# Kernel tuning notes

Hardware: AMD Instinct MI355X
Metric: run time of the kernel (lower is better)

## Reference

```python
import jax, jax.numpy as jnp
import numpy as np

NP = 16   # attention heads
HN = 128  # head dim (kv_channels)
MASK_VAL = -10000.0  # attention_mask_func fill value in TE


def setup_inputs() -> dict:
    key = jax.random.key(0)
    ks = jax.random.split(key, 5)
    S, B, H = 2048, 1, 2048
    return {
        "hidden_states": jax.random.normal(ks[0], (S, B, H), jnp.float32),
        "w_qkv": jax.random.normal(ks[1], (3 * H, H), jnp.float32) * 0.02,
        "b_qkv": jax.random.normal(ks[2], (3 * H,), jnp.float32) * 0.02,
        "w_proj": jax.random.normal(ks[3], (H, H), jnp.float32) * 0.02,
        "b_proj": jax.random.normal(ks[4], (H,), jnp.float32) * 0.02,
        "attention_mask": jnp.zeros((1, 1, S, S), dtype=bool),
    }


def reference(hidden_states, w_qkv, b_qkv, w_proj, b_proj, attention_mask):
    S, B, H = hidden_states.shape
    # fused QKV GEMM: [s, b, 3h]
    qkv = jnp.einsum("sbh,oh->sbo", hidden_states, w_qkv) + b_qkv
    qkv = qkv.reshape(S, B, NP, 3 * HN)
    q, k, v = jnp.split(qkv, 3, axis=-1)  # each [s, b, np, hn]

    # BMM1: full [b, np, sq, sk] score matrix (naive unfused attention)
    norm_factor = jnp.asarray(np.sqrt(HN), q.dtype)
    scores = jnp.einsum("sbnh,tbnh->bnst", q, k) / norm_factor

    # causal mask (attn_mask_type='causal'); provided mask OR'd in (zeros here)
    causal = jnp.triu(jnp.ones((S, S), dtype=bool), 1)
    mask = jnp.logical_or(causal, attention_mask[0, 0])
    scores = jnp.where(mask, jnp.asarray(MASK_VAL, scores.dtype), scores)

    # softmax in fp32 (apply_query_key_layer_scaling forces fp32 softmax)
    probs = jax.nn.softmax(scores.astype(jnp.float32), axis=-1).astype(q.dtype)
    # dropout p=0.0 -> identity

    # BMM2 + merge heads -> [s, b, h]
    ctx = jnp.einsum("bnst,tbnh->sbnh", probs, v).reshape(S, B, H)

    # output projection (bias returned separately, return_bias=True)
    out = jnp.einsum("sbh,oh->sbo", ctx, w_proj)
    return out, b_proj
```

## Files before the change

kernel.cpp:

```cpp
#include <hip/hip_runtime.h>
#include <math.h>

#define S_LEN   2048
#define H_DIM   2048
#define QKV_LD  6144
#define N_HEADS 16
#define HEAD_DIM 128

typedef __attribute__((ext_vector_type(8))) short short8;
typedef __attribute__((ext_vector_type(4))) float f32x4;
typedef __attribute__((ext_vector_type(16))) float f32x16;
typedef unsigned short ushort_t;

__device__ __forceinline__ ushort_t f2bf(float x) {
    unsigned int u = __float_as_uint(x);
    u = (u + 0x7fffu + ((u >> 16) & 1u)) >> 16;
    return (ushort_t)u;
}

__device__ __forceinline__ unsigned cvtpk_bf16(float a, float b) {
    unsigned r;
    asm("v_cvt_pk_bf16_f32 %0, %1, %2" : "=v"(r) : "v"(a), "v"(b));
    return r;
}

__device__ __forceinline__ void plswap(unsigned &a, unsigned &b) {
    typedef unsigned uv2 __attribute__((ext_vector_type(2)));
    uv2 r = __builtin_amdgcn_permlane32_swap(a, b, false, false);
    a = r[0]; b = r[1];
}

#define GLOBAL_LOAD_LDS16(gp, lp)                                              \
    __builtin_amdgcn_global_load_lds(                                          \
        (const __attribute__((address_space(1))) void*)(gp),                   \
        (__attribute__((address_space(3))) void*)(lp), 16, 0, 0)

#define MKFRAG(P, base, out) {                                                 \
    unsigned wa = cvtpk_bf16(P[(base)+0], P[(base)+1]);                        \
    unsigned wb = cvtpk_bf16(P[(base)+4], P[(base)+5]);                        \
    unsigned wc = cvtpk_bf16(P[(base)+2], P[(base)+3]);                        \
    unsigned wd = cvtpk_bf16(P[(base)+6], P[(base)+7]);                        \
    plswap(wa, wb); plswap(wc, wd);                                            \
    union { unsigned u[4]; short8 s; } fu;                                     \
    fu.u[0] = wa; fu.u[1] = wc; fu.u[2] = wb; fu.u[3] = wd;                    \
    out = fu.s; }

__global__ __launch_bounds__(256) void cvt_bf16(const float* __restrict__ src,
                                                ushort_t* __restrict__ dst) {
    const int i = (blockIdx.x * 256 + threadIdx.x) * 8;
    float4 a = *(const float4*)(src + i);
    float4 b = *(const float4*)(src + i + 4);
    short8 v;
    v[0] = f2bf(a.x); v[1] = f2bf(a.y); v[2] = f2bf(a.z); v[3] = f2bf(a.w);
    v[4] = f2bf(b.x); v[5] = f2bf(b.y); v[6] = f2bf(b.z); v[7] = f2bf(b.w);
    *(short8*)(dst + i) = v;
}

template <bool BIAS, bool OUT_BF16>
__global__ __launch_bounds__(256)
void gemm_bf16_nt(const ushort_t* __restrict__ A, const ushort_t* __restrict__ B,
                  const float* __restrict__ bias, void* __restrict__ Cout,
                  int M, int N, int K) {
    __shared__ __align__(16) ushort_t As[128 * 64];
    __shared__ __align__(16) ushort_t Bs[128 * 64];

    const int tid  = threadIdx.x;
    const int lane = tid & 63;
    const int w    = tid >> 6;
    const int wr   = w >> 1, wc = w & 1;
    const int m0   = blockIdx.y << 7;
    const int n0   = blockIdx.x << 7;
    const int frow = lane & 15;
    const int fk16 = (lane >> 4) << 4;

    f32x4 acc[4][4];
    #pragma unroll
    for (int i = 0; i < 4; i++)
        #pragma unroll
        for (int j = 0; j < 4; j++) acc[i][j] = (f32x4){0.f, 0.f, 0.f, 0.f};

    for (int k0 = 0; k0 < K; k0 += 64) {
        __syncthreads();
        #pragma unroll
        for (int i = 0; i < 4; i++) {
            const int off = (i * 256 + tid) * 8;
            const int r   = off >> 6;
            const int cb  = ((off & 63) * 2) ^ ((r & 7) << 4);
            GLOBAL_LOAD_LDS16((const char*)(A + (size_t)(m0 + r) * K + k0) + cb,
                              (char*)As + off * 2);
            GLOBAL_LOAD_LDS16((const char*)(B + (size_t)(n0 + r) * K + k0) + cb,
                              (char*)Bs + off * 2);
        }
        __syncthreads();
        #pragma unroll
        for (int kk = 0; kk < 2; kk++) {
            short8 a[4], b[4];
            #pragma unroll
            for (int mi = 0; mi < 4; mi++) {
                const int row = wr * 64 + mi * 16 + frow;
                const int cb  = (kk * 64 + fk16) ^ ((row & 7) << 4);
                a[mi] = *(const short8*)((const char*)As + row * 128 + cb);
            }
            #pragma unroll
            for (int ni = 0; ni < 4; ni++) {
                const int row = wc * 64 + ni * 16 + frow;
                const int cb  = (kk * 64 + fk16) ^ ((row & 7) << 4);
                b[ni] = *(const short8*)((const char*)Bs + row * 128 + cb);
            }
            #pragma unroll
            for (int mi = 0; mi < 4; mi++)
                #pragma unroll
                for (int ni = 0; ni < 4; ni++)
                    acc[mi][ni] = __builtin_amdgcn_mfma_f32_16x16x32_bf16(
                        a[mi], b[ni], acc[mi][ni], 0, 0, 0);
        }
    }

    const int crow0 = (lane >> 4) * 4;
    const int ccol  = lane & 15;
    #pragma unroll
    for (int mi = 0; mi < 4; mi++) {
        #pragma unroll
        for (int ni = 0; ni < 4; ni++) {
            const int col = n0 + wc * 64 + ni * 16 + ccol;
            const float bv = BIAS ? bias[col] : 0.f;
            #pragma unroll
            for (int r = 0; r < 4; r++) {
                const int row = m0 + wr * 64 + mi * 16 + crow0 + r;
                const float v = acc[mi][ni][r] + bv;
                if (OUT_BF16)
                    ((ushort_t*)Cout)[(size_t)row * N + col] = f2bf(v);
                else
                    ((float*)Cout)[(size_t)row * N + col] = v;
            }
        }
    }
}

__global__ __launch_bounds__(128)
void attn_mfma2(const ushort_t* __restrict__ qkv, ushort_t* __restrict__ ctx)
{
    __shared__ __align__(16) ushort_t Ks[2][64 * 128];
    __shared__ __align__(16) ushort_t Vt[2][128 * 72];

    const int tid  = threadIdx.x;
    const int lane = tid & 63;
    const int w    = tid >> 6;
    const int b    = blockIdx.x;
    const int head = blockIdx.y;
    const int l31  = lane & 31;
    const int hi   = lane >> 5;
    const size_t hbase = (size_t)head * 384;
    const ushort_t* kbase = qkv + hbase + 128;
    const ushort_t* vbase = qkv + hbase + 256;
    const int kq = tid & 15;
    const int dc = tid >> 4;

    short8 vreg[8];

    auto stage_k = [&](int kt, ushort_t* dst) {
        const int krow0 = kt << 6;
        #pragma unroll
        for (int i = 0; i < 8; i++) {
            const int off  = (i * 128 + tid) * 8;
            const int r    = off >> 7;
            const int slot = (off & 127) >> 3;
            const int sb   = (slot ^ (r & 15)) << 4;
            GLOBAL_LOAD_LDS16(
                (const char*)(kbase + (size_t)(krow0 + r) * QKV_LD) + sb,
                (char*)dst + off * 2);
        }
    };
    auto load_v = [&](int kt) {
        const int k0 = kt << 6;
        #pragma unroll
        for (int kk = 0; kk < 4; kk++)
            #pragma unroll
            for (int h2 = 0; h2 < 2; h2++)
                vreg[kk * 2 + h2] = *(const short8*)(vbase +
                    (size_t)(k0 + 4 * kq + kk) * QKV_LD + dc * 16 + h2 * 8);
    };
    auto write_vt = [&](ushort_t* dst) {
        #pragma unroll
        for (int j = 0; j < 16; j++) {
            const int h2 = j >> 3, e = j & 7;
            unsigned lo = (unsigned)(unsigned short)vreg[0 + h2][e] |
                          ((unsigned)(unsigned short)vreg[2 + h2][e] << 16);
            unsigned hh = (unsigned)(unsigned short)vreg[4 + h2][e] |
                          ((unsigned)(unsigned short)vreg[6 + h2][e] << 16);
            unsigned long long v64 =
                (unsigned long long)lo | ((unsigned long long)hh << 32);
            *(unsigned long long*)(dst + (dc * 16 + j) * 72 + 4 * kq) = v64;
        }
    };

    #pragma unroll 1
    for (int phase = 0; phase < 2; phase++) {
        const int qt = (phase == 0) ? (2 * b + w) : (63 - 2 * b - w);
        const int nt = (phase == 0) ? (b + 1) : (32 - b);
        const int q  = qt * 32 + l31;

        short8 qf[8];
        const ushort_t* qrow = qkv + (size_t)q * QKV_LD + hbase;
        #pragma unroll
        for (int ks = 0; ks < 8; ks++)
            qf[ks] = *(const short8*)(qrow + ks * 16 + hi * 8);

        f32x16 accO[4];
        #pragma unroll
        for (int dt = 0; dt < 4; dt++)
            #pragma unroll
            for (int i = 0; i < 16; i++) accO[dt][i] = 0.f;
        float m_run = -INFINITY, l_run = 0.f;

        stage_k(0, Ks[0]);
        load_v(0);
        __syncthreads();
        write_vt(Vt[0]);
        __syncthreads();

        for (int kt = 0; kt < nt; kt++) {
            const int cur = kt & 1;
            const ushort_t* Kc = Ks[cur];
            const ushort_t* Vc = Vt[cur];
            const bool pre = (kt + 1 < nt);
            if (pre) { stage_k(kt + 1, Ks[cur ^ 1]); load_v(kt + 1); }

            f32x16 s0, s1;
            #pragma unroll
            for (int i = 0; i < 16; i++) { s0[i] = 0.f; s1[i] = 0.f; }
            __builtin_amdgcn_s_setprio(1);
            #pragma unroll
            for (int ks = 0; ks < 8; ks++) {
                const int sb = (((2 * ks + hi) ^ (l31 & 15)) << 4);
                short8 kf0 = *(const short8*)((const char*)Kc + l31 * 256 + sb);
                short8 kf1 = *(const short8*)((const char*)Kc + (32 + l31) * 256 + sb);
                s0 = __builtin_amdgcn_mfma_f32_32x32x16_bf16(kf0, qf[ks], s0, 0, 0, 0);
                s1 = __builtin_amdgcn_mfma_f32_32x32x16_bf16(kf1, qf[ks], s1, 0, 0, 0);
            }
            __builtin_amdgcn_s_setprio(0);

            const float norm = 0.08838834764831843f;
            const int k0g = kt * 64;
            float p0[16], p1[16];
            #pragma unroll
            for (int r = 0; r < 16; r++) {
                const int kp = (r & 3) + 8 * (r >> 2) + 4 * hi;
                float v0 = s0[r] * norm;
                float v1 = s1[r] * norm;
                if (kt == nt - 1) {
                    if (k0g + kp > q)      v0 = -INFINITY;
                    if (k0g + 32 + kp > q) v1 = -INFINITY;
                }
                p0[r] = v0; p1[r] = v1;
            }
            float mx = fmaxf(p0[0], p1[0]);
            #pragma unroll
            for (int r = 1; r < 16; r++) mx = fmaxf(mx, fmaxf(p0[r], p1[r]));
            mx = fmaxf(mx, __shfl_xor(mx, 32));
            const float mnew = fmaxf(m_run, mx);
            float ps = 0.f;
            #pragma unroll
            for (int r = 0; r < 16; r++) {
                p0[r] = __expf(p0[r] - mnew);
                p1[r] = __expf(p1[r] - mnew);
                ps += p0[r] + p1[r];
            }
            ps += __shfl_xor(ps, 32);
            const float sc = __expf(m_run - mnew);
            l_run = l_run * sc + ps;
            m_run = mnew;
            #pragma unroll
            for (int dt = 0; dt < 4; dt++)
                #pragma unroll
                for (int i = 0; i < 16; i++) accO[dt][i] *= sc;

            short8 pf[4];
            MKFRAG(p0, 0, pf[0]); MKFRAG(p0, 8, pf[1]);
            MKFRAG(p1, 0, pf[2]); MKFRAG(p1, 8, pf[3]);

            if (pre) write_vt(Vt[cur ^ 1]);

            __builtin_amdgcn_s_setprio(1);
            #pragma unroll
            for (int dt = 0; dt < 4; dt++)
                #pragma unroll
                for (int ks = 0; ks < 4; ks++) {
                    short8 vf = *(const short8*)(Vc + (dt * 32 + l31) * 72 +
                                                 ks * 16 + hi * 8);
                    accO[dt] = __builtin_amdgcn_mfma_f32_32x32x16_bf16(
                        vf, pf[ks], accO[dt], 0, 0, 0);
                }
            __builtin_amdgcn_s_setprio(0);
            __syncthreads();
        }

        const float inv = 1.f / l_run;
        ushort_t* crow = ctx + (size_t)q * H_DIM + head * HEAD_DIM;
        #pragma unroll
        for (int dblk = 0; dblk < 8; dblk++) {
            const int dt = dblk >> 1;
            const int base = (dblk & 1) * 8;
            unsigned wa = cvtpk_bf16(accO[dt][base + 0] * inv, accO[dt][base + 1] * inv);
            unsigned wb = cvtpk_bf16(accO[dt][base + 4] * inv, accO[dt][base + 5] * inv);
            unsigned wc = cvtpk_bf16(accO[dt][base + 2] * inv, accO[dt][base + 3] * inv);
            unsigned wd = cvtpk_bf16(accO[dt][base + 6] * inv, accO[dt][base + 7] * inv);
            plswap(wa, wb); plswap(wc, wd);
            union { unsigned u[4]; short8 s; } fu;
            fu.u[0] = wa; fu.u[1] = wc; fu.u[2] = wb; fu.u[3] = wd;
            *(short8*)(crow + dblk * 16 + hi * 8) = fu.s;
        }
    }
}

__global__ __launch_bounds__(256) void copy_bias(const float* __restrict__ b,
                                                 float* __restrict__ out) {
    const int i = blockIdx.x * 256 + threadIdx.x;
    if (i < H_DIM) out[i] = b[i];
}

extern "C" void kernel_launch(void* const* d_in, const int* in_sizes, int n_in,
                              void* d_out, int out_size, void* d_ws, size_t ws_size,
                              hipStream_t stream) {
    const float* hidden = (const float*)d_in[0];
    const float* w_qkv  = (const float*)d_in[1];
    const float* b_qkv  = (const float*)d_in[2];
    const float* w_proj = (const float*)d_in[3];
    const float* b_proj = (const float*)d_in[4];
    float* out = (float*)d_out;

    ushort_t* qkvb = (ushort_t*)d_ws;
    ushort_t* bufB = qkvb + (size_t)S_LEN * QKV_LD;
    ushort_t* bufC = bufB + (size_t)S_LEN * H_DIM;

    cvt_bf16<<<dim3((S_LEN * H_DIM) / 2048), 256, 0, stream>>>(hidden, bufB);
    cvt_bf16<<<dim3((QKV_LD * H_DIM) / 2048), 256, 0, stream>>>(w_qkv, bufC);

    gemm_bf16_nt<true, true><<<dim3(QKV_LD / 128, S_LEN / 128), 256, 0, stream>>>(
        bufB, bufC, b_qkv, qkvb, S_LEN, QKV_LD, H_DIM);

    cvt_bf16<<<dim3((H_DIM * H_DIM) / 2048), 256, 0, stream>>>(w_proj, bufC);

    attn_mfma2<<<dim3(16, N_HEADS), 128, 0, stream>>>(qkvb, bufB);

    gemm_bf16_nt<false, false><<<dim3(H_DIM / 128, S_LEN / 128), 256, 0, stream>>>(
        bufB, bufC, nullptr, out, S_LEN, H_DIM, H_DIM);

    copy_bias<<<dim3((H_DIM + 255) / 256), 256, 0, stream>>>(
        b_proj, out + (size_t)S_LEN * H_DIM);
}
```

Measured before the change: 356.2 us.

## Pre-transpose V, triple-buffer async K/V staging in attention, shrink proj GEMM tile

A separate kernel now transposes V into a per-head [d, s] buffer in workspace. The attention kernel can then load both K and V tiles straight into LDS with async global-to-LDS copies, instead of loading V into registers and transposing it in shared memory. The attention loop uses a three-stage ring buffer with explicit vmcnt waits and raw barriers, so two tiles are prefetched ahead of compute, and its grid is reordered to head-major. The output projection GEMM gets a templated BM=64 tile, doubling its block count for better CU occupancy. In exchange there is an extra kernel launch, an extra pass over V through memory, and more LDS per attention block.

```diff
diff --git a/kernel.cpp b/kernel.cpp
--- a/kernel.cpp
+++ b/kernel.cpp
@@ -56,48 +56,82 @@
     *(short8*)(dst + i) = v;
 }
 
-template <bool BIAS, bool OUT_BF16>
+__global__ __launch_bounds__(256)
+void vt_transpose(const ushort_t* __restrict__ qkv, ushort_t* __restrict__ vt) {
+    __shared__ ushort_t T[64 * 72];
+    const int tid  = threadIdx.x;
+    const int s0   = blockIdx.x << 6;
+    const int d0   = blockIdx.y << 6;
+    const int head = blockIdx.z;
+    const ushort_t* src = qkv + (size_t)head * 384 + 256;
+    #pragma unroll
+    for (int j = 0; j < 2; j++) {
+        const int idx = j * 256 + tid;
+        const int r = idx >> 3, c = idx & 7;
+        *(short8*)&T[r * 72 + c * 8] =
+            *(const short8*)(src + (size_t)(s0 + r) * QKV_LD + d0 + c * 8);
+    }
+    __syncthreads();
+    #pragma unroll
+    for (int j = 0; j < 2; j++) {
+        const int idx = j * 256 + tid;
+        const int dr = idx >> 3, sc = idx & 7;
+        short8 v;
+        #pragma unroll
+        for (int e = 0; e < 8; e++) v[e] = T[(sc * 8 + e) * 72 + dr];
+        *(short8*)(vt + ((size_t)head * HEAD_DIM + d0 + dr) * S_LEN + s0 + sc * 8) = v;
+    }
+}
+
+template <int BM, bool BIAS, bool OUT_BF16>
 __global__ __launch_bounds__(256)
 void gemm_bf16_nt(const ushort_t* __restrict__ A, const ushort_t* __restrict__ B,
                   const float* __restrict__ bias, void* __restrict__ Cout,
                   int M, int N, int K) {
-    __shared__ __align__(16) ushort_t As[128 * 64];
+    constexpr int MI = BM / 32;
+    __shared__ __align__(16) ushort_t As[BM * 64];
     __shared__ __align__(16) ushort_t Bs[128 * 64];
 
     const int tid  = threadIdx.x;
     const int lane = tid & 63;
     const int w    = tid >> 6;
     const int wr   = w >> 1, wc = w & 1;
-    const int m0   = blockIdx.y << 7;
+    const int m0   = blockIdx.y * BM;
     const int n0   = blockIdx.x << 7;
     const int frow = lane & 15;
     const int fk16 = (lane >> 4) << 4;
 
-    f32x4 acc[4][4];
+    f32x4 acc[MI][4];
     #pragma unroll
-    for (int i = 0; i < 4; i++)
+    for (int i = 0; i < MI; i++)
         #pragma unroll
         for (int j = 0; j < 4; j++) acc[i][j] = (f32x4){0.f, 0.f, 0.f, 0.f};
 
     for (int k0 = 0; k0 < K; k0 += 64) {
         __syncthreads();
         #pragma unroll
-        for (int i = 0; i < 4; i++) {
+        for (int i = 0; i < MI; i++) {
             const int off = (i * 256 + tid) * 8;
             const int r   = off >> 6;
             const int cb  = ((off & 63) * 2) ^ ((r & 7) << 4);
             GLOBAL_LOAD_LDS16((const char*)(A + (size_t)(m0 + r) * K + k0) + cb,
                               (char*)As + off * 2);
+        }
+        #pragma unroll
+        for (int i = 0; i < 4; i++) {
+            const int off = (i * 256 + tid) * 8;
+            const int r   = off >> 6;
+            const int cb  = ((off & 63) * 2) ^ ((r & 7) << 4);
             GLOBAL_LOAD_LDS16((const char*)(B + (size_t)(n0 + r) * K + k0) + cb,
                               (char*)Bs + off * 2);
         }
         __syncthreads();
         #pragma unroll
         for (int kk = 0; kk < 2; kk++) {
-            short8 a[4], b[4];
-            #pragma unroll
-            for (int mi = 0; mi < 4; mi++) {
-                const int row = wr * 64 + mi * 16 + frow;
+            short8 a[MI], b[4];
+            #pragma unroll
+            for (int mi = 0; mi < MI; mi++) {
+                const int row = wr * (BM / 2) + mi * 16 + frow;
                 const int cb  = (kk * 64 + fk16) ^ ((row & 7) << 4);
                 a[mi] = *(const short8*)((const char*)As + row * 128 + cb);
             }
@@ -108,7 +142,7 @@
                 b[ni] = *(const short8*)((const char*)Bs + row * 128 + cb);
             }
             #pragma unroll
-            for (int mi = 0; mi < 4; mi++)
+            for (int mi = 0; mi < MI; mi++)
                 #pragma unroll
                 for (int ni = 0; ni < 4; ni++)
                     acc[mi][ni] = __builtin_amdgcn_mfma_f32_16x16x32_bf16(
@@ -119,14 +153,14 @@
     const int crow0 = (lane >> 4) * 4;
     const int ccol  = lane & 15;
     #pragma unroll
-    for (int mi = 0; mi < 4; mi++) {
+    for (int mi = 0; mi < MI; mi++) {
         #pragma unroll
         for (int ni = 0; ni < 4; ni++) {
             const int col = n0 + wc * 64 + ni * 16 + ccol;
             const float bv = BIAS ? bias[col] : 0.f;
             #pragma unroll
             for (int r = 0; r < 4; r++) {
-                const int row = m0 + wr * 64 + mi * 16 + crow0 + r;
+                const int row = m0 + wr * (BM / 2) + mi * 16 + crow0 + r;
                 const float v = acc[mi][ni][r] + bv;
                 if (OUT_BF16)
                     ((ushort_t*)Cout)[(size_t)row * N + col] = f2bf(v);
@@ -138,59 +172,42 @@
 }
 
 __global__ __launch_bounds__(128)
-void attn_mfma2(const ushort_t* __restrict__ qkv, ushort_t* __restrict__ ctx)
+void attn_mfma3(const ushort_t* __restrict__ qkv, const ushort_t* __restrict__ vt,
+                ushort_t* __restrict__ ctx)
 {
-    __shared__ __align__(16) ushort_t Ks[2][64 * 128];
-    __shared__ __align__(16) ushort_t Vt[2][128 * 72];
+    __shared__ __align__(16) ushort_t Ks[3][64 * 128];
+    __shared__ __align__(16) ushort_t Vs[3][128 * 64];
 
     const int tid  = threadIdx.x;
     const int lane = tid & 63;
     const int w    = tid >> 6;
-    const int b    = blockIdx.x;
-    const int head = blockIdx.y;
+    const int head = blockIdx.x;
+    const int b    = blockIdx.y;
     const int l31  = lane & 31;
     const int hi   = lane >> 5;
     const size_t hbase = (size_t)head * 384;
     const ushort_t* kbase = qkv + hbase + 128;
-    const ushort_t* vbase = qkv + hbase + 256;
-    const int kq = tid & 15;
-    const int dc = tid >> 4;
-
-    short8 vreg[8];
-
-    auto stage_k = [&](int kt, ushort_t* dst) {
-        const int krow0 = kt << 6;
+    const ushort_t* vtb   = vt + (size_t)head * HEAD_DIM * S_LEN;
+
+    auto stage = [&](int t, int s) {
+        const int k0 = t << 6;
+        char* kd = (char*)Ks[s];
+        char* vd = (char*)Vs[s];
         #pragma unroll
         for (int i = 0; i < 8; i++) {
-            const int off  = (i * 128 + tid) * 8;
-            const int r    = off >> 7;
-            const int slot = (off & 127) >> 3;
-            const int sb   = (slot ^ (r & 15)) << 4;
+            const int idx = w * 512 + i * 64 + lane;
+            const int r = idx >> 4, sl = idx & 15;
             GLOBAL_LOAD_LDS16(
-                (const char*)(kbase + (size_t)(krow0 + r) * QKV_LD) + sb,
-                (char*)dst + off * 2);
-        }
-    };
-    auto load_v = [&](int kt) {
-        const int k0 = kt << 6;
-        #pragma unroll
-        for (int kk = 0; kk < 4; kk++)
-            #pragma unroll
-            for (int h2 = 0; h2 < 2; h2++)
-                vreg[kk * 2 + h2] = *(const short8*)(vbase +
-                    (size_t)(k0 + 4 * kq + kk) * QKV_LD + dc * 16 + h2 * 8);
-    };
-    auto write_vt = [&](ushort_t* dst) {
-        #pragma unroll
-        for (int j = 0; j < 16; j++) {
-            const int h2 = j >> 3, e = j & 7;
-            unsigned lo = (unsigned)(unsigned short)vreg[0 + h2][e] |
-                          ((unsigned)(unsigned short)vreg[2 + h2][e] << 16);
-            unsigned hh = (unsigned)(unsigned short)vreg[4 + h2][e] |
-                          ((unsigned)(unsigned short)vreg[6 + h2][e] << 16);
-            unsigned long long v64 =
-                (unsigned long long)lo | ((unsigned long long)hh << 32);
-            *(unsigned long long*)(dst + (dc * 16 + j) * 72 + 4 * kq) = v64;
+                (const char*)(kbase + (size_t)(k0 + r) * QKV_LD) + ((sl ^ (r & 15)) << 4),
+                kd + idx * 16);
+        }
+        #pragma unroll
+        for (int i = 0; i < 8; i++) {
+            const int idx = w * 512 + i * 64 + lane;
+            const int r = idx >> 3, sl = idx & 7;
+            GLOBAL_LOAD_LDS16(
+                (const char*)(vtb + (size_t)r * S_LEN + k0) + ((sl ^ (r & 7)) << 4),
+                vd + idx * 16);
         }
     };
 
@@ -213,18 +230,25 @@
             for (int i = 0; i < 16; i++) accO[dt][i] = 0.f;
         float m_run = -INFINITY, l_run = 0.f;
 
-        stage_k(0, Ks[0]);
-        load_v(0);
-        __syncthreads();
-        write_vt(Vt[0]);
-        __syncthreads();
-
+        stage(0, 0);
+        if (nt > 1) stage(1, 1);
+
+        int cur = 0;
         for (int kt = 0; kt < nt; kt++) {
-            const int cur = kt & 1;
+            const int rem = nt - 1 - kt;
+            if (rem >= 2) {
+                int s2 = cur - 1; if (s2 < 0) s2 = 2;
+                stage(kt + 2, s2);
+                asm volatile("s_waitcnt vmcnt(32)" ::: "memory");
+            } else if (rem == 1) {
+                asm volatile("s_waitcnt vmcnt(16)" ::: "memory");
+            } else {
+                asm volatile("s_waitcnt vmcnt(0)" ::: "memory");
+            }
+            __builtin_amdgcn_s_barrier();
+
             const ushort_t* Kc = Ks[cur];
-            const ushort_t* Vc = Vt[cur];
-            const bool pre = (kt + 1 < nt);
-            if (pre) { stage_k(kt + 1, Ks[cur ^ 1]); load_v(kt + 1); }
+            const ushort_t* Vc = Vs[cur];
 
             f32x16 s0, s1;
             #pragma unroll
@@ -279,20 +303,20 @@
             MKFRAG(p0, 0, pf[0]); MKFRAG(p0, 8, pf[1]);
             MKFRAG(p1, 0, pf[2]); MKFRAG(p1, 8, pf[3]);
 
-            if (pre) write_vt(Vt[cur ^ 1]);
-
             __builtin_amdgcn_s_setprio(1);
             #pragma unroll
             for (int dt = 0; dt < 4; dt++)
                 #pragma unroll
                 for (int ks = 0; ks < 4; ks++) {
-                    short8 vf = *(const short8*)(Vc + (dt * 32 + l31) * 72 +
-                                                 ks * 16 + hi * 8);
+                    const int vrow = dt * 32 + l31;
+                    short8 vf = *(const short8*)((const char*)Vc + vrow * 128 +
+                                  (((ks * 2 + hi) ^ (vrow & 7)) << 4));
                     accO[dt] = __builtin_amdgcn_mfma_f32_32x32x16_bf16(
                         vf, pf[ks], accO[dt], 0, 0, 0);
                 }
             __builtin_amdgcn_s_setprio(0);
-            __syncthreads();
+            __builtin_amdgcn_s_barrier();
+            cur = (cur == 2) ? 0 : cur + 1;
         }
 
         const float inv = 1.f / l_run;
@@ -329,21 +353,24 @@
     const float* b_proj = (const float*)d_in[4];
     float* out = (float*)d_out;
 
-    ushort_t* qkvb = (ushort_t*)d_ws;
-    ushort_t* bufB = qkvb + (size_t)S_LEN * QKV_LD;
-    ushort_t* bufC = bufB + (size_t)S_LEN * H_DIM;
+    ushort_t* qkvb  = (ushort_t*)d_ws;
+    ushort_t* bufB  = qkvb + (size_t)S_LEN * QKV_LD;
+    ushort_t* bufC  = bufB + (size_t)S_LEN * H_DIM;
+    ushort_t* vtbuf = bufC + (size_t)QKV_LD * H_DIM;
 
     cvt_bf16<<<dim3((S_LEN * H_DIM) / 2048), 256, 0, stream>>>(hidden, bufB);
     cvt_bf16<<<dim3((QKV_LD * H_DIM) / 2048), 256, 0, stream>>>(w_qkv, bufC);
 
-    gemm_bf16_nt<true, true><<<dim3(QKV_LD / 128, S_LEN / 128), 256, 0, stream>>>(
+    gemm_bf16_nt<128, true, true><<<dim3(QKV_LD / 128, S_LEN / 128), 256, 0, stream>>>(
         bufB, bufC, b_qkv, qkvb, S_LEN, QKV_LD, H_DIM);
 
+    vt_transpose<<<dim3(S_LEN / 64, 2, N_HEADS), 256, 0, stream>>>(qkvb, vtbuf);
+
     cvt_bf16<<<dim3((H_DIM * H_DIM) / 2048), 256, 0, stream>>>(w_proj, bufC);
 
-    attn_mfma2<<<dim3(16, N_HEADS), 128, 0, stream>>>(qkvb, bufB);
-
-    gemm_bf16_nt<false, false><<<dim3(H_DIM / 128, S_LEN / 128), 256, 0, stream>>>(
+    attn_mfma3<<<dim3(N_HEADS, 16), 128, 0, stream>>>(qkvb, vtbuf, bufB);
+
+    gemm_bf16_nt<64, false, false><<<dim3(H_DIM / 128, S_LEN / 64), 256, 0, stream>>>(
         bufB, bufC, nullptr, out, S_LEN, H_DIM, H_DIM);
 
     copy_bias<<<dim3((H_DIM + 255) / 256), 256, 0, stream>>>(
```

Result: faster. 336.5 us (-5.5%).
